# Performance work log

Hardware: AMD Instinct MI355X
Metric: run time of the kernel (lower is better)

## Reference

```python
import jax, jax.numpy as jnp
import numpy as np


def _conv(x, w, b, pad):
    y = jax.lax.conv_general_dilated(x, w, (1, 1), [(pad, pad), (pad, pad)],
                                     dimension_numbers=('NCHW', 'OIHW', 'NCHW'))
    return y + b[None, :, None, None]


def _pool(x):
    return jax.lax.reduce_window(x, -jnp.inf, jax.lax.max, (1, 1, 2, 2), (1, 1, 2, 2), 'VALID')


def _up(x):
    return jnp.repeat(jnp.repeat(x, 2, axis=2), 2, axis=3)


def _unet(x, p):
    r = jax.nn.relu
    e1 = r(_conv(x, p['enc1_w'], p['enc1_b'], 1))                            # [B,16,H,W]
    e2 = r(_conv(_pool(e1), p['enc2_w'], p['enc2_b'], 1))                    # [B,32,H/2,W/2]
    bt = r(_conv(_pool(e2), p['bott_w'], p['bott_b'], 1))                    # [B,64,H/4,W/4]
    d2 = r(_conv(jnp.concatenate([_up(bt), e2], 1), p['dec2_w'], p['dec2_b'], 1))
    d1 = r(_conv(jnp.concatenate([_up(d2), e1], 1), p['dec1_w'], p['dec1_b'], 1))
    return _conv(d1, p['out_w'], p['out_b'], 0)                              # [B,C,H,W]


def _global_match(ref_e, cur_e):
    # FEELVOS global matching: for each current-frame pixel, distance to the
    # nearest reference-frame pixel in embedding space, mapped through
    # d = 1 - 2/(1+exp(||e_p - e_q||^2)). Monotone, so apply after the min.
    N, E, H, W = ref_e.shape
    a = ref_e.reshape(N, E, H * W).transpose(0, 2, 1)   # [N, P, E] reference pixels
    b = cur_e.reshape(N, E, H * W).transpose(0, 2, 1)   # [N, Q, E] current pixels
    d2 = (jnp.sum(a * a, -1)[:, :, None] + jnp.sum(b * b, -1)[:, None, :]
          - 2.0 * jnp.einsum('npe,nqe->npq', a, b))     # [N, P, Q]
    dmin = jnp.min(jnp.maximum(d2, 0.0), axis=1)        # [N, Q] nearest-neighbor dist^2
    return (1.0 - 2.0 * jax.nn.sigmoid(-dmin)).reshape(N, 1, H, W)


def setup_inputs() -> dict:
    key = jax.random.key(0)
    ks = jax.random.split(key, 16)
    B, C, H, W, CIN = 2, 4, 48, 48, 3

    def w(k, shape):
        fan_in = int(np.prod(shape[1:]))
        return jax.random.normal(k, shape, jnp.float32) * np.float32(1.0 / np.sqrt(fan_in))

    return {
        'x1': jax.random.uniform(ks[0], (B, C, H, W), jnp.float32),
        'x2': jax.random.uniform(ks[1], (B, C, H, W), jnp.float32),
        'x3': jax.random.normal(ks[2], (B, CIN, H, W), jnp.float32),
        'enc1_w': w(ks[3], (16, CIN, 3, 3)), 'enc1_b': jnp.zeros((16,), jnp.float32),
        'enc2_w': w(ks[4], (32, 16, 3, 3)), 'enc2_b': jnp.zeros((32,), jnp.float32),
        'bott_w': w(ks[5], (64, 32, 3, 3)), 'bott_b': jnp.zeros((64,), jnp.float32),
        'dec2_w': w(ks[6], (32, 96, 3, 3)), 'dec2_b': jnp.zeros((32,), jnp.float32),
        'dec1_w': w(ks[7], (16, 48, 3, 3)), 'dec1_b': jnp.zeros((16,), jnp.float32),
        'out_w': w(ks[8], (C, 16, 1, 1)), 'out_b': jnp.zeros((C,), jnp.float32),
        'emb_w': w(ks[9], (100, 1, 3, 3)), 'emb_b': jnp.zeros((100,), jnp.float32),
        'dsh_w': w(ks[10], (1, C + 3, 3, 3)), 'dsh_b': jnp.zeros((1,), jnp.float32),
    }


def reference(x1, x2, x3, enc1_w, enc1_b, enc2_w, enc2_b, bott_w, bott_b,
              dec2_w, dec2_b, dec1_w, dec1_b, out_w, out_b, emb_w, emb_b,
              dsh_w, dsh_b):
    p = dict(enc1_w=enc1_w, enc1_b=enc1_b, enc2_w=enc2_w, enc2_b=enc2_b,
             bott_w=bott_w, bott_b=bott_b, dec2_w=dec2_w, dec2_b=dec2_b,
             dec1_w=dec1_w, dec1_b=dec1_b, out_w=out_w, out_b=out_b)
    B, C, H, W = x1.shape
    x3s = _unet(x3, p)                        # backbone on current frame -> [B,C,H,W]
    # fold the per-class Python loop into the batch axis (shared weights)
    x1f = x1.reshape(B * C, 1, H, W)
    x2f = x2.reshape(B * C, 1, H, W)
    x3f = x3s.reshape(B * C, 1, H, W)
    e1 = _conv(x1f, emb_w, emb_b, 1)          # [B*C,100,H,W]
    e2 = _conv(x2f, emb_w, emb_b, 1)
    e3 = _conv(x3f, emb_w, emb_b, 1)
    gm = _global_match(e1, e3)                # first-frame matching  [B*C,1,H,W]
    lm = _global_match(e2, e3)                # previous-frame matching
    x3rep = jnp.broadcast_to(x3s[:, None], (B, C, C, H, W)).reshape(B * C, C, H, W)
    x_t = jnp.concatenate([x3rep, gm, lm, x2f], axis=1)   # [B*C, C+3, H, W]
    logits = _conv(x_t, dsh_w, dsh_b, 1).reshape(B, C, H, W)
    # faithful to the original final loop: output is cat(logits[C-2], logits[C-1])
    return jnp.concatenate([logits[:, C - 2:C - 1], logits[:, C - 1:C]], axis=1)
```

## Files before the change

### kernel.cpp

```cpp
#include <hip/hip_runtime.h>
#include <math.h>

#define THREADS 256
#define HW 2304

typedef __attribute__((ext_vector_type(8))) short short8;
typedef __attribute__((ext_vector_type(4))) float f32x4;
typedef __attribute__((ext_vector_type(8))) unsigned short us8;

typedef const __attribute__((address_space(1))) void* gas_p;
typedef __attribute__((address_space(3))) void* las_p;

__device__ __forceinline__ void gll16(const void* g, const void* l) {
    __builtin_amdgcn_global_load_lds((gas_p)g, (las_p)l, 16, 0, 0);
}

__device__ __forceinline__ void stage_rows(const float* __restrict__ src, float* __restrict__ dst,
                                           int nch, int chStride, int H, int W,
                                           int rlo, int rcount, int tid, int nthr, bool relu) {
    int rowfl = W + 4;
    int total = nch * rcount * rowfl;
    float4 z = make_float4(0.f, 0.f, 0.f, 0.f);
    for (int i = tid; i * 4 < total; i += nthr) ((float4*)dst)[i] = z;
    __syncthreads();
    int w2 = W >> 1;
    int m = nch * rcount * w2;
    for (int i = tid; i < m; i += nthr) {
        int c2 = i % w2;
        int rr = (i / w2) % rcount;
        int ch = i / (w2 * rcount);
        int srow = rlo + rr;
        if (srow < 0 || srow >= H) continue;
        float2 v = *(const float2*)(src + (size_t)ch * chStride + srow * W + 2 * c2);
        if (relu) { v.x = fmaxf(v.x, 0.f); v.y = fmaxf(v.y, 0.f); }
        *(float2*)(dst + (size_t)ch * rcount * rowfl + rr * rowfl + 2 + 2 * c2) = v;
    }
    __syncthreads();
}

#define LOAD_W9(wlbase, ci)                                        \
    const float4* wp4 = (const float4*)((wlbase) + (ci) * 12);     \
    float4 wa = wp4[0], wb = wp4[1], wc = wp4[2];                  \
    const float w9[9] = {wa.x, wa.y, wa.z, wa.w, wb.x, wb.y, wb.z, wb.w, wc.x};

__global__ void k_init(float* __restrict__ d2b, float* __restrict__ d1b,
                       const float* __restrict__ b2, const float* __restrict__ b1) {
    int idx = blockIdx.x * THREADS + threadIdx.x;
    if (idx < 36864) {
        d2b[idx] = b2[(idx / 576) & 31];
    } else if (idx < 110592) {
        int j = idx - 36864;
        d1b[j] = b1[(j / HW) & 15];
    }
}

__global__ __launch_bounds__(192) void k_enc1pool(const float* __restrict__ x3, const float* __restrict__ w,
                                                  const float* __restrict__ b, float* __restrict__ e1u,
                                                  float* __restrict__ p1) {
    int co = blockIdx.x & 15, n = blockIdx.x >> 4;
    int tid = threadIdx.x;
    __shared__ __align__(16) float lds[3 * 50 * 52];
    __shared__ __align__(16) float wl[48];
    for (int i = tid; i < 27; i += 192) wl[(i / 9) * 12 + (i % 9)] = w[(co * 3) * 9 + i];
    stage_rows(x3 + (size_t)n * 3 * HW, lds, 3, HW, 48, 48, -1, 50, tid, 192, false);
    float bv = b[co];
    for (int o = 0; o < 3; ++o) {
        int po = o * 192 + tid;
        int py = po / 24, px = po % 24;
        float s[2][2] = {{bv, bv}, {bv, bv}};
        for (int ci = 0; ci < 3; ++ci) {
            const float* chp = lds + ci * 2600;
            float c[4][6];
            #pragma unroll
            for (int rr = 0; rr < 4; ++rr) {
                const float2* pr = (const float2*)(chp + (2 * py + rr) * 52);
                #pragma unroll
                for (int k = 0; k < 3; ++k) { float2 t = pr[px + k]; c[rr][2 * k] = t.x; c[rr][2 * k + 1] = t.y; }
            }
            LOAD_W9(wl, ci)
            #pragma unroll
            for (int dy = 0; dy < 3; ++dy)
                #pragma unroll
                for (int dx = 0; dx < 3; ++dx) {
                    float wv = w9[dy * 3 + dx];
                    #pragma unroll
                    for (int yy = 0; yy < 2; ++yy)
                        #pragma unroll
                        for (int xx = 0; xx < 2; ++xx)
                            s[yy][xx] = fmaf(c[yy + dy][xx + dx + 1], wv, s[yy][xx]);
                }
        }
        float* ob = e1u + (size_t)(n * 16 + co) * HW;
        float mx = -INFINITY;
        #pragma unroll
        for (int yy = 0; yy < 2; ++yy)
            #pragma unroll
            for (int xx = 0; xx < 2; ++xx) {
                float v = fmaxf(s[yy][xx], 0.f);
                ob[(2 * py + yy) * 48 + 2 * px + xx] = v;
                mx = fmaxf(mx, v);
            }
        p1[(size_t)(n * 16 + co) * 576 + py * 24 + px] = mx;
    }
}

__global__ __launch_bounds__(192) void k_enc2pool(const float* __restrict__ p1, const float* __restrict__ w,
                                                  const float* __restrict__ b, float* __restrict__ e2,
                                                  float* __restrict__ p2) {
    int co = blockIdx.x & 31, n = blockIdx.x >> 5;
    int tid = threadIdx.x;
    __shared__ __align__(16) float lds[16 * 26 * 28];
    __shared__ __align__(16) float wl[192];
    for (int i = tid; i < 144; i += 192) wl[(i / 9) * 12 + (i % 9)] = w[(co * 16) * 9 + i];
    stage_rows(p1 + (size_t)n * 16 * 576, lds, 16, 576, 24, 24, -1, 26, tid, 192, false);
    if (tid < 144) {
        int py = tid / 12, px = tid % 12;
        float bv = b[co];
        float s[2][2] = {{bv, bv}, {bv, bv}};
        for (int ci = 0; ci < 16; ++ci) {
            const float* chp = lds + ci * 728;
            float c[4][6];
            #pragma unroll
            for (int rr = 0; rr < 4; ++rr) {
                const float2* pr = (const float2*)(chp + (2 * py + rr) * 28);
                #pragma unroll
                for (int k = 0; k < 3; ++k) { float2 t = pr[px + k]; c[rr][2 * k] = t.x; c[rr][2 * k + 1] = t.y; }
            }
            LOAD_W9(wl, ci)
            #pragma unroll
            for (int dy = 0; dy < 3; ++dy)
                #pragma unroll
                for (int dx = 0; dx < 3; ++dx) {
                    float wv = w9[dy * 3 + dx];
                    #pragma unroll
                    for (int yy = 0; yy < 2; ++yy)
                        #pragma unroll
                        for (int xx = 0; xx < 2; ++xx)
                            s[yy][xx] = fmaf(c[yy + dy][xx + dx + 1], wv, s[yy][xx]);
                }
        }
        float* ob = e2 + (size_t)(n * 32 + co) * 576;
        float mx = -INFINITY;
        #pragma unroll
        for (int yy = 0; yy < 2; ++yy)
            #pragma unroll
            for (int xx = 0; xx < 2; ++xx) {
                float v = fmaxf(s[yy][xx], 0.f);
                ob[(2 * py + yy) * 24 + 2 * px + xx] = v;
                mx = fmaxf(mx, v);
            }
        p2[(size_t)(n * 32 + co) * 144 + py * 12 + px] = mx;
    }
}

__global__ __launch_bounds__(192) void k_bott(const float* __restrict__ p2, const float* __restrict__ w,
                                              const float* __restrict__ b, float* __restrict__ bt) {
    int co = blockIdx.x & 63, n = blockIdx.x >> 6;
    int tid = threadIdx.x;
    __shared__ __align__(16) float lds[32 * 14 * 16];
    __shared__ __align__(16) float wl[384];
    for (int i = tid; i < 288; i += 192) wl[(i / 9) * 12 + (i % 9)] = w[(co * 32) * 9 + i];
    stage_rows(p2 + (size_t)n * 32 * 144, lds, 32, 144, 12, 12, -1, 14, tid, 192, false);
    if (tid < 144) {
        int y = tid / 12, x = tid % 12;
        float acc = b[co];
        for (int ci = 0; ci < 32; ++ci) {
            const float* chp = lds + ci * 224;
            LOAD_W9(wl, ci)
            #pragma unroll
            for (int dy = 0; dy < 3; ++dy)
                #pragma unroll
                for (int dx = 0; dx < 3; ++dx)
                    acc = fmaf(chp[(y + dy) * 16 + x + dx + 1], w9[dy * 3 + dx], acc);
        }
        bt[(size_t)(n * 64 + co) * 144 + y * 12 + x] = fmaxf(acc, 0.f);
    }
}

__global__ __launch_bounds__(192) void k_dec2p(const float* __restrict__ bt, const float* __restrict__ e2,
                                               const float* __restrict__ w, float* __restrict__ d2b) {
    int bx = blockIdx.x;
    int chunk = bx & 3, co = (bx >> 2) & 31, n = bx >> 7;
    int cib = chunk * 24;
    int nA = max(0, min(24, 64 - cib));
    int nB = 24 - nA;
    int tid = threadIdx.x;
    __shared__ __align__(16) float lds[24 * 26 * 28];
    __shared__ __align__(16) float wl[288];
    for (int i = tid; i < 216; i += 192) wl[(i / 9) * 12 + (i % 9)] = w[((size_t)co * 96 + cib) * 9 + i];
    stage_rows(bt + ((size_t)n * 64 + cib) * 144, lds, nA, 144, 12, 12, -1, 14, tid, 192, false);
    float* ldsB = lds + nA * 224;
    int e2c = max(0, cib + nA - 64);
    stage_rows(e2 + ((size_t)n * 32 + e2c) * 576, ldsB, nB, 576, 24, 24, -1, 26, tid, 192, false);
    if (tid < 144) {
        int y = tid / 6, qx = tid % 6;
        float acc[4] = {0.f, 0.f, 0.f, 0.f};
        int r0 = ((y - 1) >> 1) + 1;
        int yodd = y & 1;
        for (int ci = 0; ci < nA; ++ci) {
            const float* chp = lds + ci * 224;
            const float2* p0 = (const float2*)(chp + r0 * 16);
            const float2* p1 = (const float2*)(chp + (r0 + 1) * 16);
            float a0[6], a1[6], am[6];
            #pragma unroll
            for (int k = 0; k < 3; ++k) {
                float2 t0 = p0[qx + k], t1 = p1[qx + k];
                a0[2 * k] = t0.x; a0[2 * k + 1] = t0.y;
                a1[2 * k] = t1.x; a1[2 * k + 1] = t1.y;
            }
            #pragma unroll
            for (int k = 0; k < 6; ++k) am[k] = yodd ? a0[k] : a1[k];
            LOAD_W9(wl, ci)
            #pragma unroll
            for (int dy = 0; dy < 3; ++dy) {
                const float* rr = (dy == 0) ? a0 : (dy == 1 ? am : a1);
                #pragma unroll
                for (int dx = 0; dx < 3; ++dx) {
                    float wv = w9[dy * 3 + dx];
                    #pragma unroll
                    for (int j = 0; j < 4; ++j)
                        acc[j] = fmaf(rr[((j + dx - 1) >> 1) + 2], wv, acc[j]);
                }
            }
        }
        for (int ci = 0; ci < nB; ++ci) {
            const float* chp = ldsB + ci * 728;
            float bvv[3][8];
            #pragma unroll
            for (int r = 0; r < 3; ++r) {
                const float2* pr = (const float2*)(chp + (y + r) * 28);
                #pragma unroll
                for (int k = 0; k < 4; ++k) { float2 t = pr[2 * qx + k]; bvv[r][2 * k] = t.x; bvv[r][2 * k + 1] = t.y; }
            }
            LOAD_W9(wl, nA + ci)
            #pragma unroll
            for (int dy = 0; dy < 3; ++dy)
                #pragma unroll
                for (int dx = 0; dx < 3; ++dx) {
                    float wv = w9[dy * 3 + dx];
                    #pragma unroll
                    for (int j = 0; j < 4; ++j)
                        acc[j] = fmaf(bvv[dy][j + dx + 1], wv, acc[j]);
                }
        }
        float* op = d2b + ((size_t)(n * 32 + co)) * 576 + y * 24 + qx * 4;
        #pragma unroll
        for (int j = 0; j < 4; ++j) atomicAdd(op + j, acc[j]);
    }
}

__global__ __launch_bounds__(192) void k_dec1p(const float* __restrict__ d2b, const float* __restrict__ e1u,
                                               const float* __restrict__ w, float* __restrict__ d1b) {
    int bx = blockIdx.x;
    int strip = bx % 3;
    int chunk = (bx / 3) & 3;
    int co = (bx / 12) & 15;
    int n = bx / 192;
    int cib = chunk * 12;
    int nA = max(0, min(12, 32 - cib));
    int nB = 12 - nA;
    int y0 = strip * 16;
    int yhlo = (y0 - 1) >> 1;
    int tid = threadIdx.x;
    __shared__ __align__(16) float lds[12 * 18 * 52];
    __shared__ __align__(16) float wl[144];
    for (int i = tid; i < 108; i += 192) wl[(i / 9) * 12 + (i % 9)] = w[((size_t)co * 48 + cib) * 9 + i];
    stage_rows(d2b + ((size_t)n * 32 + cib) * 576, lds, nA, 576, 24, 24, yhlo, 10, tid, 192, true);
    float* ldsB = lds + nA * 280;
    int e1c = max(0, cib + nA - 32);
    stage_rows(e1u + ((size_t)n * 16 + e1c) * HW, ldsB, nB, HW, 48, 48, y0 - 1, 18, tid, 192, false);
    {
        int yl = tid / 12, qx = tid % 12;
        int y = y0 + yl;
        float acc[4] = {0.f, 0.f, 0.f, 0.f};
        int r0 = ((y - 1) >> 1) - yhlo;
        int yodd = y & 1;
        for (int ci = 0; ci < nA; ++ci) {
            const float* chp = lds + ci * 280;
            const float2* p0 = (const float2*)(chp + r0 * 28);
            const float2* p1 = (const float2*)(chp + (r0 + 1) * 28);
            float a0[6], a1[6], am[6];
            #pragma unroll
            for (int k = 0; k < 3; ++k) {
                float2 t0 = p0[qx + k], t1 = p1[qx + k];
                a0[2 * k] = t0.x; a0[2 * k + 1] = t0.y;
                a1[2 * k] = t1.x; a1[2 * k + 1] = t1.y;
            }
            #pragma unroll
            for (int k = 0; k < 6; ++k) am[k] = yodd ? a0[k] : a1[k];
            LOAD_W9(wl, ci)
            #pragma unroll
            for (int dy = 0; dy < 3; ++dy) {
                const float* rr = (dy == 0) ? a0 : (dy == 1 ? am : a1);
                #pragma unroll
                for (int dx = 0; dx < 3; ++dx) {
                    float wv = w9[dy * 3 + dx];
                    #pragma unroll
                    for (int j = 0; j < 4; ++j)
                        acc[j] = fmaf(rr[((j + dx - 1) >> 1) + 2], wv, acc[j]);
                }
            }
        }
        for (int ci = 0; ci < nB; ++ci) {
            const float* chp = ldsB + ci * 936;
            float bvv[3][8];
            #pragma unroll
            for (int r = 0; r < 3; ++r) {
                const float2* pr = (const float2*)(chp + (yl + r) * 52);
                #pragma unroll
                for (int k = 0; k < 4; ++k) { float2 t = pr[2 * qx + k]; bvv[r][2 * k] = t.x; bvv[r][2 * k + 1] = t.y; }
            }
            LOAD_W9(wl, nA + ci)
            #pragma unroll
            for (int dy = 0; dy < 3; ++dy)
                #pragma unroll
                for (int dx = 0; dx < 3; ++dx) {
                    float wv = w9[dy * 3 + dx];
                    #pragma unroll
                    for (int j = 0; j < 4; ++j)
                        acc[j] = fmaf(bvv[dy][j + dx + 1], wv, acc[j]);
                }
        }
        float* op = d1b + ((size_t)(n * 16 + co)) * HW + y * 48 + qx * 4;
        #pragma unroll
        for (int j = 0; j < 4; ++j) atomicAdd(op + j, acc[j]);
    }
}

__global__ void k_out1x1(const float* __restrict__ d1b, const float* __restrict__ ow,
                         const float* __restrict__ ob, float* __restrict__ x3s) {
    int idx = blockIdx.x * THREADS + threadIdx.x;
    if (idx >= 18432) return;
    int q = idx % HW;
    int co = (idx / HW) & 3;
    int n = idx / 9216;
    float acc = ob[co];
    #pragma unroll
    for (int ci = 0; ci < 16; ++ci)
        acc = fmaf(fmaxf(d1b[((size_t)(n * 16 + ci)) * HW + q], 0.f), ow[co * 16 + ci], acc);
    x3s[((size_t)(n * 4 + co)) * HW + q] = acc;
}

__global__ __launch_bounds__(THREADS) void k_embprep(
        const float* __restrict__ x1, const float* __restrict__ x2,
        const float* __restrict__ x3s, const float* __restrict__ ew,
        const float* __restrict__ eb, unsigned short* __restrict__ hl,
        float* __restrict__ nrm, unsigned* __restrict__ initbuf) {
    int bx = blockIdx.x;
    int tid = threadIdx.x;
    if (bx >= 108) {
        int i = (bx - 108) * THREADS + tid;
        if (i < 2 * 4 * HW) initbuf[i] = 0x7F800000u;
        return;
    }
    int pt = bx % 9, ni = (bx / 9) % 4, arr = bx / 36;
    int plane = 2 + (ni & 1) + 4 * (ni >> 1);
    const float* src = (arr == 0 ? x1 : (arr == 1 ? x2 : x3s)) + (size_t)plane * HW;

    __shared__ float wl[1300];
    for (int i = tid; i < 900; i += THREADS) wl[(i / 9) * 12 + (i % 9)] = ew[i];
    for (int i = tid; i < 100; i += THREADS) wl[1200 + i] = eb[i];
    __syncthreads();

    int pix = pt * THREADS + tid;
    int x = pix % 48, y = pix / 48;
    float p9[9];
    #pragma unroll
    for (int ky = 0; ky < 3; ++ky)
        #pragma unroll
        for (int kx = 0; kx < 3; ++kx) {
            int yy = y + ky - 1, xx = x + kx - 1;
            p9[ky * 3 + kx] = (yy >= 0 && yy < 48 && xx >= 0 && xx < 48) ? src[yy * 48 + xx] : 0.f;
        }

    float nsum = 0.f;
    char* rowp = (char*)(hl + (((size_t)(arr * 4 + ni)) * HW + pix) * 256);
    for (int g = 0; g < 16; ++g) {
        us8 vh, vl;
        #pragma unroll
        for (int j = 0; j < 8; ++j) {
            int e = g * 8 + j;
            float v = 0.f;
            if (e < 100) {
                v = wl[1200 + e];
                #pragma unroll
                for (int k = 0; k < 9; ++k) v = fmaf(p9[k], wl[e * 12 + k], v);
                nsum = fmaf(v, v, nsum);
            }
            unsigned bits = __float_as_uint(v);
            vh[j] = (unsigned short)(bits >> 16);
            float lo = v - __uint_as_float(bits & 0xFFFF0000u);
            vl[j] = (unsigned short)(__float_as_uint(lo) >> 16);
        }
        *(us8*)(rowp + g * 16) = vh;
        *(us8*)(rowp + 256 + g * 16) = vl;
    }
    nrm[(size_t)(arr * 4 + ni) * HW + pix] = nsum;
}

__global__ __launch_bounds__(THREADS) void k_match(
        const unsigned short* __restrict__ hl, const float* __restrict__ nrm,
        unsigned* __restrict__ gmd, unsigned* __restrict__ lmd) {
    int bx = blockIdx.x;
    int ps = bx % 3;
    int rest = bx / 3;
    int qt = rest % 18;
    int n = (rest / 18) % 4;
    int m = rest / 72;

    const unsigned short* curhl = hl + ((size_t)(8 + n)) * HW * 256;
    const unsigned short* refhl = hl + ((size_t)(m * 4 + n)) * HW * 256;
    const float* na = nrm + (size_t)(m * 4 + n) * HW;
    const float* nb = nrm + (size_t)(8 + n) * HW;
    unsigned* outd = (m == 0 ? gmd : lmd) + (size_t)n * HW;

    int qbase = qt * 128;
    int pbase = ps * 768;

    __shared__ unsigned short lds[(128 + 32) * 256];
    unsigned short* curl = lds;
    unsigned short* refl = lds + 128 * 256;

    int tid = threadIdx.x;
    int wave = tid >> 6;
    int lane = tid & 63;
    int lr = lane >> 5;
    int lc = lane & 31;

    {
        const unsigned short* gb = curhl + (size_t)qbase * 256;
        for (int t = 0; t < 16; ++t) {
            int i = wave * 16 + t;
            int r = 2 * i + lr;
            int sc = lc ^ (r & 7);
            gll16(gb + (size_t)r * 256 + sc * 8, curl + i * 512);
        }
    }
    __syncthreads();

    short8 ahi[2][4], alo[2][4];
    #pragma unroll
    for (int j = 0; j < 2; ++j) {
        int r = wave * 32 + j * 16 + (lane & 15);
        #pragma unroll
        for (int ks = 0; ks < 4; ++ks) {
            int cg = ks * 4 + (lane >> 4);
            const char* p = (const char*)curl + r * 512 + ((cg ^ (r & 7)) << 4);
            ahi[j][ks] = *(const short8*)p;
            alo[j][ks] = *(const short8*)(p + 256);
        }
    }

    float dmin[2][4];
    #pragma unroll
    for (int j = 0; j < 2; ++j)
        #pragma unroll
        for (int r = 0; r < 4; ++r) dmin[j][r] = INFINITY;

    for (int pc = 0; pc < 24; ++pc) {
        __syncthreads();
        {
            const unsigned short* gb = refhl + (size_t)(pbase + pc * 32) * 256;
            for (int t = 0; t < 4; ++t) {
                int i = wave * 4 + t;
                int r = 2 * i + lr;
                int sc = lc ^ (r & 7);
                gll16(gb + (size_t)r * 256 + sc * 8, refl + i * 512);
            }
        }
        __syncthreads();

        short8 bhi[2][4], blo[2][4];
        #pragma unroll
        for (int ptile = 0; ptile < 2; ++ptile) {
            int r = ptile * 16 + (lane & 15);
            #pragma unroll
            for (int ks = 0; ks < 4; ++ks) {
                int cg = ks * 4 + (lane >> 4);
                const char* p = (const char*)refl + r * 512 + ((cg ^ (r & 7)) << 4);
                bhi[ptile][ks] = *(const short8*)p;
                blo[ptile][ks] = *(const short8*)(p + 256);
            }
        }

        f32x4 acc[2][2];
        #pragma unroll
        for (int ptile = 0; ptile < 2; ++ptile)
            #pragma unroll
            for (int j = 0; j < 2; ++j) acc[ptile][j] = (f32x4){0.f, 0.f, 0.f, 0.f};

        #pragma unroll
        for (int ks = 0; ks < 4; ++ks) {
            #pragma unroll
            for (int ptile = 0; ptile < 2; ++ptile)
                #pragma unroll
                for (int j = 0; j < 2; ++j)
                    acc[ptile][j] = __builtin_amdgcn_mfma_f32_16x16x32_bf16(
                        ahi[j][ks], bhi[ptile][ks], acc[ptile][j], 0, 0, 0);
            #pragma unroll
            for (int ptile = 0; ptile < 2; ++ptile)
                #pragma unroll
                for (int j = 0; j < 2; ++j)
                    acc[ptile][j] = __builtin_amdgcn_mfma_f32_16x16x32_bf16(
                        ahi[j][ks], blo[ptile][ks], acc[ptile][j], 0, 0, 0);
            #pragma unroll
            for (int ptile = 0; ptile < 2; ++ptile)
                #pragma unroll
                for (int j = 0; j < 2; ++j)
                    acc[ptile][j] = __builtin_amdgcn_mfma_f32_16x16x32_bf16(
                        alo[j][ks], bhi[ptile][ks], acc[ptile][j], 0, 0, 0);
        }

        #pragma unroll
        for (int ptile = 0; ptile < 2; ++ptile) {
            float nav = na[pbase + pc * 32 + ptile * 16 + (lane & 15)];
            #pragma unroll
            for (int j = 0; j < 2; ++j)
                #pragma unroll
                for (int r = 0; r < 4; ++r)
                    dmin[j][r] = fminf(dmin[j][r], fmaf(-2.f, acc[ptile][j][r], nav));
        }
    }

    #pragma unroll
    for (int j = 0; j < 2; ++j)
        #pragma unroll
        for (int r = 0; r < 4; ++r) {
            float v = dmin[j][r];
            v = fminf(v, __shfl_xor(v, 1, 64));
            v = fminf(v, __shfl_xor(v, 2, 64));
            v = fminf(v, __shfl_xor(v, 4, 64));
            v = fminf(v, __shfl_xor(v, 8, 64));
            if ((lane & 15) == 0) {
                int q = qbase + wave * 32 + j * 16 + 4 * (lane >> 4) + r;
                float d2 = fmaxf(v + nb[q], 0.f);
                atomicMin(&outd[q], __float_as_uint(d2));
            }
        }
}

__global__ void k_final(const float* __restrict__ x3s, const unsigned* __restrict__ gmd,
                        const unsigned* __restrict__ lmd, const float* __restrict__ x2,
                        const float* __restrict__ dshw, const float* __restrict__ dshb,
                        float* __restrict__ out) {
    int idx = blockIdx.x * THREADS + threadIdx.x;
    if (idx >= 9216) return;
    int q = idx % HW, ni = idx / HW;
    int n = 2 + (ni & 1) + 4 * (ni >> 1);
    int b = ni >> 1;
    int x = q % 48, y = q / 48;
    float acc = dshb[0];
    for (int c = 0; c < 7; ++c) {
        const float* wp = dshw + c * 9;
        #pragma unroll
        for (int ky = 0; ky < 3; ++ky) {
            int yy = y + ky - 1;
            if (yy < 0 || yy >= 48) continue;
            #pragma unroll
            for (int kx = 0; kx < 3; ++kx) {
                int xx = x + kx - 1;
                if (xx < 0 || xx >= 48) continue;
                float v;
                if (c < 4) v = x3s[(size_t)(b * 4 + c) * HW + yy * 48 + xx];
                else if (c == 4) {
                    float d2 = __uint_as_float(gmd[(size_t)ni * HW + yy * 48 + xx]);
                    v = 1.f - 2.f / (1.f + expf(d2));
                } else if (c == 5) {
                    float d2 = __uint_as_float(lmd[(size_t)ni * HW + yy * 48 + xx]);
                    v = 1.f - 2.f / (1.f + expf(d2));
                } else v = x2[(size_t)n * HW + yy * 48 + xx];
                acc = fmaf(v, wp[ky * 3 + kx], acc);
            }
        }
    }
    out[idx] = acc;
}

extern "C" void kernel_launch(void* const* d_in, const int* in_sizes, int n_in,
                              void* d_out, int out_size, void* d_ws, size_t ws_size,
                              hipStream_t stream) {
    const float* x1     = (const float*)d_in[0];
    const float* x2     = (const float*)d_in[1];
    const float* x3     = (const float*)d_in[2];
    const float* enc1_w = (const float*)d_in[3];
    const float* enc1_b = (const float*)d_in[4];
    const float* enc2_w = (const float*)d_in[5];
    const float* enc2_b = (const float*)d_in[6];
    const float* bott_w = (const float*)d_in[7];
    const float* bott_b = (const float*)d_in[8];
    const float* dec2_w = (const float*)d_in[9];
    const float* dec2_b = (const float*)d_in[10];
    const float* dec1_w = (const float*)d_in[11];
    const float* dec1_b = (const float*)d_in[12];
    const float* out_w  = (const float*)d_in[13];
    const float* out_b  = (const float*)d_in[14];
    const float* emb_w  = (const float*)d_in[15];
    const float* emb_b  = (const float*)d_in[16];
    const float* dsh_w  = (const float*)d_in[17];
    const float* dsh_b  = (const float*)d_in[18];

    float* w = (float*)d_ws;
    float* e1u  = w;
    float* p1   = w + 73728;
    float* e2   = w + 92160;
    float* p2   = w + 129024;
    float* bt   = w + 138240;
    float* d2b  = w + 156672;
    float* d1b  = w + 193536;
    float* x3s  = w + 267264;
    float* nrm  = w + 285696;
    unsigned* gmd = (unsigned*)(w + 313344);
    unsigned* lmd = (unsigned*)(w + 322560);
    unsigned short* hl = (unsigned short*)(w + 331776);

    k_init<<<dim3(432), dim3(THREADS), 0, stream>>>(d2b, d1b, dec2_b, dec1_b);
    k_enc1pool<<<dim3(32), dim3(192), 0, stream>>>(x3, enc1_w, enc1_b, e1u, p1);
    k_enc2pool<<<dim3(64), dim3(192), 0, stream>>>(p1, enc2_w, enc2_b, e2, p2);
    k_bott<<<dim3(128), dim3(192), 0, stream>>>(p2, bott_w, bott_b, bt);
    k_dec2p<<<dim3(256), dim3(192), 0, stream>>>(bt, e2, dec2_w, d2b);
    k_dec1p<<<dim3(384), dim3(192), 0, stream>>>(d2b, e1u, dec1_w, d1b);
    k_out1x1<<<dim3(72), dim3(THREADS), 0, stream>>>(d1b, out_w, out_b, x3s);
    k_embprep<<<dim3(180), dim3(THREADS), 0, stream>>>(x1, x2, x3s, emb_w, emb_b, hl, nrm, gmd);
    k_match<<<dim3(432), dim3(THREADS), 0, stream>>>(hl, nrm, gmd, lmd);
    k_final<<<dim3(36), dim3(THREADS), 0, stream>>>(x3s, gmd, lmd, x2, dsh_w, dsh_b, (float*)d_out);
}
```

Before: 148.8 us.

## Fuse init, enc1 and x1/x2 embedding into one kernel; double-buffer match loads

The bias init, enc1+pool, the x1/x2 embedding prep and the atomicMin buffer init are merged into one launch, and only the x3s embedding stays after the backbone. This removes a launch and lets the independent embedding work run alongside enc1. In k_match, the current-frame tile is read straight from global into registers instead of staged in LDS. Reference tiles are double-buffered with async global-to-LDS loads and waitcnt, norms are cached in LDS, and blocks are remapped across XCDs. The tradeoff is a larger combined LDS footprint in k_pre and a fragile hand-written vmcnt/barrier sync.

```diff
diff --git a/kernel.cpp b/kernel.cpp
--- a/kernel.cpp
+++ b/kernel.cpp
@@ -43,29 +43,91 @@
     float4 wa = wp4[0], wb = wp4[1], wc = wp4[2];                  \
     const float w9[9] = {wa.x, wa.y, wa.z, wa.w, wb.x, wb.y, wb.z, wb.w, wc.x};
 
-__global__ void k_init(float* __restrict__ d2b, float* __restrict__ d1b,
-                       const float* __restrict__ b2, const float* __restrict__ b1) {
-    int idx = blockIdx.x * THREADS + threadIdx.x;
-    if (idx < 36864) {
-        d2b[idx] = b2[(idx / 576) & 31];
-    } else if (idx < 110592) {
-        int j = idx - 36864;
-        d1b[j] = b1[(j / HW) & 15];
-    }
-}
-
-__global__ __launch_bounds__(192) void k_enc1pool(const float* __restrict__ x3, const float* __restrict__ w,
-                                                  const float* __restrict__ b, float* __restrict__ e1u,
-                                                  float* __restrict__ p1) {
-    int co = blockIdx.x & 15, n = blockIdx.x >> 4;
+__device__ __forceinline__ void emb_body(const float* __restrict__ src, int arr, int ni, int pt,
+                                         const float* __restrict__ ew, const float* __restrict__ eb,
+                                         unsigned short* __restrict__ hl, float* __restrict__ nrm,
+                                         float* wl, int tid, int nthr) {
+    for (int i = tid; i < 900; i += nthr) wl[(i / 9) * 12 + (i % 9)] = ew[i];
+    for (int i = tid; i < 100; i += nthr) wl[1200 + i] = eb[i];
+    __syncthreads();
+
+    int pix = pt * 256 + tid;
+    int x = pix % 48, y = pix / 48;
+    float p9[9];
+    #pragma unroll
+    for (int ky = 0; ky < 3; ++ky)
+        #pragma unroll
+        for (int kx = 0; kx < 3; ++kx) {
+            int yy = y + ky - 1, xx = x + kx - 1;
+            p9[ky * 3 + kx] = (yy >= 0 && yy < 48 && xx >= 0 && xx < 48) ? src[yy * 48 + xx] : 0.f;
+        }
+
+    float nsum = 0.f;
+    char* rowp = (char*)(hl + (((size_t)(arr * 4 + ni)) * HW + pix) * 256);
+    for (int g = 0; g < 16; ++g) {
+        us8 vh, vl;
+        #pragma unroll
+        for (int j = 0; j < 8; ++j) {
+            int e = g * 8 + j;
+            float v = 0.f;
+            if (e < 100) {
+                v = wl[1200 + e];
+                #pragma unroll
+                for (int k = 0; k < 9; ++k) v = fmaf(p9[k], wl[e * 12 + k], v);
+                nsum = fmaf(v, v, nsum);
+            }
+            unsigned bits = __float_as_uint(v);
+            vh[j] = (unsigned short)(bits >> 16);
+            float lo = v - __uint_as_float(bits & 0xFFFF0000u);
+            vl[j] = (unsigned short)(__float_as_uint(lo) >> 16);
+        }
+        *(us8*)(rowp + g * 16) = vh;
+        *(us8*)(rowp + 256 + g * 16) = vl;
+    }
+    nrm[(size_t)(arr * 4 + ni) * HW + pix] = nsum;
+}
+
+__global__ __launch_bounds__(256) void k_pre(
+        float* __restrict__ d2b, float* __restrict__ d1b,
+        const float* __restrict__ b2, const float* __restrict__ b1,
+        const float* __restrict__ x1, const float* __restrict__ x2,
+        const float* __restrict__ ew, const float* __restrict__ eb,
+        unsigned short* __restrict__ hl, float* __restrict__ nrm,
+        unsigned* __restrict__ initbuf,
+        const float* __restrict__ x3, const float* __restrict__ e1w,
+        const float* __restrict__ e1b, float* __restrict__ e1u, float* __restrict__ p1) {
+    __shared__ __align__(16) float lds[3 * 50 * 52];
+    __shared__ __align__(16) float wl1[48];
+    __shared__ float wl[1300];
+    int bx = blockIdx.x;
     int tid = threadIdx.x;
-    __shared__ __align__(16) float lds[3 * 50 * 52];
-    __shared__ __align__(16) float wl[48];
-    for (int i = tid; i < 27; i += 192) wl[(i / 9) * 12 + (i % 9)] = w[(co * 3) * 9 + i];
-    stage_rows(x3 + (size_t)n * 3 * HW, lds, 3, HW, 48, 48, -1, 50, tid, 192, false);
-    float bv = b[co];
+    if (bx < 432) {
+        int idx = bx * 256 + tid;
+        if (idx < 36864) d2b[idx] = b2[(idx / 576) & 31];
+        else d1b[idx - 36864] = b1[((idx - 36864) / HW) & 15];
+        return;
+    }
+    if (bx < 504) {
+        int sub = bx - 432;
+        int arr = sub / 36;
+        int ni = (sub % 36) / 9, pt = sub % 9;
+        int plane = 2 + (ni & 1) + 4 * (ni >> 1);
+        const float* src = (arr == 0 ? x1 : x2) + (size_t)plane * HW;
+        emb_body(src, arr, ni, pt, ew, eb, hl, nrm, wl, tid, 256);
+        return;
+    }
+    if (bx < 576) {
+        int i = (bx - 504) * 256 + tid;
+        initbuf[i] = 0x7F800000u;
+        return;
+    }
+    int co = (bx - 576) & 15, n = (bx - 576) >> 4;
+    for (int i = tid; i < 27; i += 256) wl1[(i / 9) * 12 + (i % 9)] = e1w[(co * 3) * 9 + i];
+    stage_rows(x3 + (size_t)n * 3 * HW, lds, 3, HW, 48, 48, -1, 50, tid, 256, false);
+    float bv = e1b[co];
     for (int o = 0; o < 3; ++o) {
-        int po = o * 192 + tid;
+        int po = o * 256 + tid;
+        if (po >= 576) break;
         int py = po / 24, px = po % 24;
         float s[2][2] = {{bv, bv}, {bv, bv}};
         for (int ci = 0; ci < 3; ++ci) {
@@ -77,7 +139,7 @@
                 #pragma unroll
                 for (int k = 0; k < 3; ++k) { float2 t = pr[px + k]; c[rr][2 * k] = t.x; c[rr][2 * k + 1] = t.y; }
             }
-            LOAD_W9(wl, ci)
+            LOAD_W9(wl1, ci)
             #pragma unroll
             for (int dy = 0; dy < 3; ++dy)
                 #pragma unroll
@@ -341,72 +403,26 @@
     x3s[((size_t)(n * 4 + co)) * HW + q] = acc;
 }
 
-__global__ __launch_bounds__(THREADS) void k_embprep(
-        const float* __restrict__ x1, const float* __restrict__ x2,
-        const float* __restrict__ x3s, const float* __restrict__ ew,
-        const float* __restrict__ eb, unsigned short* __restrict__ hl,
-        float* __restrict__ nrm, unsigned* __restrict__ initbuf) {
-    int bx = blockIdx.x;
-    int tid = threadIdx.x;
-    if (bx >= 108) {
-        int i = (bx - 108) * THREADS + tid;
-        if (i < 2 * 4 * HW) initbuf[i] = 0x7F800000u;
-        return;
-    }
-    int pt = bx % 9, ni = (bx / 9) % 4, arr = bx / 36;
+__global__ __launch_bounds__(256) void k_emb3(const float* __restrict__ x3s,
+                                              const float* __restrict__ ew, const float* __restrict__ eb,
+                                              unsigned short* __restrict__ hl, float* __restrict__ nrm) {
+    __shared__ float wl[1300];
+    int ni = blockIdx.x / 9, pt = blockIdx.x % 9;
     int plane = 2 + (ni & 1) + 4 * (ni >> 1);
-    const float* src = (arr == 0 ? x1 : (arr == 1 ? x2 : x3s)) + (size_t)plane * HW;
-
-    __shared__ float wl[1300];
-    for (int i = tid; i < 900; i += THREADS) wl[(i / 9) * 12 + (i % 9)] = ew[i];
-    for (int i = tid; i < 100; i += THREADS) wl[1200 + i] = eb[i];
-    __syncthreads();
-
-    int pix = pt * THREADS + tid;
-    int x = pix % 48, y = pix / 48;
-    float p9[9];
-    #pragma unroll
-    for (int ky = 0; ky < 3; ++ky)
-        #pragma unroll
-        for (int kx = 0; kx < 3; ++kx) {
-            int yy = y + ky - 1, xx = x + kx - 1;
-            p9[ky * 3 + kx] = (yy >= 0 && yy < 48 && xx >= 0 && xx < 48) ? src[yy * 48 + xx] : 0.f;
-        }
-
-    float nsum = 0.f;
-    char* rowp = (char*)(hl + (((size_t)(arr * 4 + ni)) * HW + pix) * 256);
-    for (int g = 0; g < 16; ++g) {
-        us8 vh, vl;
-        #pragma unroll
-        for (int j = 0; j < 8; ++j) {
-            int e = g * 8 + j;
-            float v = 0.f;
-            if (e < 100) {
-                v = wl[1200 + e];
-                #pragma unroll
-                for (int k = 0; k < 9; ++k) v = fmaf(p9[k], wl[e * 12 + k], v);
-                nsum = fmaf(v, v, nsum);
-            }
-            unsigned bits = __float_as_uint(v);
-            vh[j] = (unsigned short)(bits >> 16);
-            float lo = v - __uint_as_float(bits & 0xFFFF0000u);
-            vl[j] = (unsigned short)(__float_as_uint(lo) >> 16);
-        }
-        *(us8*)(rowp + g * 16) = vh;
-        *(us8*)(rowp + 256 + g * 16) = vl;
-    }
-    nrm[(size_t)(arr * 4 + ni) * HW + pix] = nsum;
-}
-
-__global__ __launch_bounds__(THREADS) void k_match(
+    emb_body(x3s + (size_t)plane * HW, 2, ni, pt, ew, eb, hl, nrm, wl, threadIdx.x, 256);
+}
+
+#define NPC 24
+__global__ __launch_bounds__(256, 2) void k_match(
         const unsigned short* __restrict__ hl, const float* __restrict__ nrm,
         unsigned* __restrict__ gmd, unsigned* __restrict__ lmd) {
     int bx = blockIdx.x;
-    int ps = bx % 3;
-    int rest = bx / 3;
-    int qt = rest % 18;
-    int n = (rest / 18) % 4;
-    int m = rest / 72;
+    int l = (bx & 7) * 54 + (bx >> 3);
+    int ps = l % 3;
+    int qt = (l / 3) % 18;
+    int mn = l / 54;
+    int n = mn & 3;
+    int m = mn >> 2;
 
     const unsigned short* curhl = hl + ((size_t)(8 + n)) * HW * 256;
     const unsigned short* refhl = hl + ((size_t)(m * 4 + n)) * HW * 256;
@@ -417,9 +433,8 @@
     int qbase = qt * 128;
     int pbase = ps * 768;
 
-    __shared__ unsigned short lds[(128 + 32) * 256];
-    unsigned short* curl = lds;
-    unsigned short* refl = lds + 128 * 256;
+    __shared__ __align__(16) unsigned short refl[2][32 * 256];
+    __shared__ __align__(16) float nal[768];
 
     int tid = threadIdx.x;
     int wave = tid >> 6;
@@ -427,29 +442,31 @@
     int lr = lane >> 5;
     int lc = lane & 31;
 
-    {
-        const unsigned short* gb = curhl + (size_t)qbase * 256;
-        for (int t = 0; t < 16; ++t) {
-            int i = wave * 16 + t;
-            int r = 2 * i + lr;
-            int sc = lc ^ (r & 7);
-            gll16(gb + (size_t)r * 256 + sc * 8, curl + i * 512);
-        }
-    }
-    __syncthreads();
+    if (tid < 192) *(float4*)&nal[tid * 4] = *(const float4*)(na + pbase + tid * 4);
 
     short8 ahi[2][4], alo[2][4];
     #pragma unroll
     for (int j = 0; j < 2; ++j) {
-        int r = wave * 32 + j * 16 + (lane & 15);
+        int r = qbase + wave * 32 + j * 16 + (lane & 15);
+        const unsigned short* rp = curhl + (size_t)r * 256;
         #pragma unroll
         for (int ks = 0; ks < 4; ++ks) {
-            int cg = ks * 4 + (lane >> 4);
-            const char* p = (const char*)curl + r * 512 + ((cg ^ (r & 7)) << 4);
+            const unsigned short* p = rp + (ks * 4 + (lane >> 4)) * 8;
             ahi[j][ks] = *(const short8*)p;
-            alo[j][ks] = *(const short8*)(p + 256);
-        }
-    }
+            alo[j][ks] = *(const short8*)(p + 128);
+        }
+    }
+
+    {
+        const unsigned short* gb = refhl + (size_t)pbase * 256;
+        #pragma unroll
+        for (int t = 0; t < 4; ++t) {
+            int i = wave * 4 + t;
+            int r = 2 * i + lr;
+            gll16(gb + (size_t)r * 256 + (lc ^ (r & 7)) * 8, &refl[0][i * 512]);
+        }
+    }
+    asm volatile("s_waitcnt lgkmcnt(0)" ::: "memory");
 
     float dmin[2][4];
     #pragma unroll
@@ -457,18 +474,21 @@
         #pragma unroll
         for (int r = 0; r < 4; ++r) dmin[j][r] = INFINITY;
 
-    for (int pc = 0; pc < 24; ++pc) {
-        __syncthreads();
-        {
-            const unsigned short* gb = refhl + (size_t)(pbase + pc * 32) * 256;
+    for (int pc = 0; pc < NPC; ++pc) {
+        int cur = pc & 1;
+        if (pc + 1 < NPC) {
+            const unsigned short* gb = refhl + (size_t)(pbase + (pc + 1) * 32) * 256;
+            #pragma unroll
             for (int t = 0; t < 4; ++t) {
                 int i = wave * 4 + t;
                 int r = 2 * i + lr;
-                int sc = lc ^ (r & 7);
-                gll16(gb + (size_t)r * 256 + sc * 8, refl + i * 512);
-            }
-        }
-        __syncthreads();
+                gll16(gb + (size_t)r * 256 + (lc ^ (r & 7)) * 8, &refl[cur ^ 1][i * 512]);
+            }
+            asm volatile("s_waitcnt vmcnt(4)" ::: "memory");
+        } else {
+            asm volatile("s_waitcnt vmcnt(0)" ::: "memory");
+        }
+        __builtin_amdgcn_s_barrier();
 
         short8 bhi[2][4], blo[2][4];
         #pragma unroll
@@ -477,7 +497,7 @@
             #pragma unroll
             for (int ks = 0; ks < 4; ++ks) {
                 int cg = ks * 4 + (lane >> 4);
-                const char* p = (const char*)refl + r * 512 + ((cg ^ (r & 7)) << 4);
+                const char* p = (const char*)refl[cur] + r * 512 + ((cg ^ (r & 7)) << 4);
                 bhi[ptile][ks] = *(const short8*)p;
                 blo[ptile][ks] = *(const short8*)(p + 256);
             }
@@ -513,13 +533,14 @@
 
         #pragma unroll
         for (int ptile = 0; ptile < 2; ++ptile) {
-            float nav = na[pbase + pc * 32 + ptile * 16 + (lane & 15)];
+            float nav = nal[pc * 32 + ptile * 16 + (lane & 15)];
             #pragma unroll
             for (int j = 0; j < 2; ++j)
                 #pragma unroll
                 for (int r = 0; r < 4; ++r)
                     dmin[j][r] = fminf(dmin[j][r], fmaf(-2.f, acc[ptile][j][r], nav));
         }
+        __builtin_amdgcn_s_barrier();
     }
 
     #pragma unroll
@@ -613,14 +634,14 @@
     unsigned* lmd = (unsigned*)(w + 322560);
     unsigned short* hl = (unsigned short*)(w + 331776);
 
-    k_init<<<dim3(432), dim3(THREADS), 0, stream>>>(d2b, d1b, dec2_b, dec1_b);
-    k_enc1pool<<<dim3(32), dim3(192), 0, stream>>>(x3, enc1_w, enc1_b, e1u, p1);
+    k_pre<<<dim3(608), dim3(256), 0, stream>>>(d2b, d1b, dec2_b, dec1_b, x1, x2, emb_w, emb_b,
+                                               hl, nrm, gmd, x3, enc1_w, enc1_b, e1u, p1);
     k_enc2pool<<<dim3(64), dim3(192), 0, stream>>>(p1, enc2_w, enc2_b, e2, p2);
     k_bott<<<dim3(128), dim3(192), 0, stream>>>(p2, bott_w, bott_b, bt);
     k_dec2p<<<dim3(256), dim3(192), 0, stream>>>(bt, e2, dec2_w, d2b);
     k_dec1p<<<dim3(384), dim3(192), 0, stream>>>(d2b, e1u, dec1_w, d1b);
     k_out1x1<<<dim3(72), dim3(THREADS), 0, stream>>>(d1b, out_w, out_b, x3s);
-    k_embprep<<<dim3(180), dim3(THREADS), 0, stream>>>(x1, x2, x3s, emb_w, emb_b, hl, nrm, gmd);
-    k_match<<<dim3(432), dim3(THREADS), 0, stream>>>(hl, nrm, gmd, lmd);
+    k_emb3<<<dim3(36), dim3(256), 0, stream>>>(x3s, emb_w, emb_b, hl, nrm);
+    k_match<<<dim3(432), dim3(256), 0, stream>>>(hl, nrm, gmd, lmd);
     k_final<<<dim3(36), dim3(THREADS), 0, stream>>>(x3s, gmd, lmd, x2, dsh_w, dsh_b, (float*)d_out);
 }
```

After: 136.8 us. 8.1% less time.
